# Kernel optimization log

Hardware: AMD Instinct MI355X
Metric: run time of the kernel (lower is better)

## Reference

```python
import jax, jax.numpy as jnp
import numpy as np

B, N, C, H = 4, 2048, 768, 12
D = C // H  # head_dim = 64


def setup_inputs() -> dict:
    key = jax.random.key(0)
    ks = jax.random.split(key, 16)
    s = 1.0 / np.sqrt(C)
    inp = {
        "x1": jax.random.normal(ks[0], (B, N, C), jnp.float32),
        "x2": jax.random.normal(ks[1], (B, N, C), jnp.float32),
        "mask_1": jax.random.uniform(ks[2], (B, N), jnp.float32),
        "mask_2": jax.random.uniform(ks[3], (B, N), jnp.float32),
        "Wq": jax.random.normal(ks[4], (C, C), jnp.float32) * s,
        "bq": jnp.zeros((C,), jnp.float32),
        "Wk": jax.random.normal(ks[5], (C, C), jnp.float32) * s,
        "bk": jnp.zeros((C,), jnp.float32),
        "Wv": jax.random.normal(ks[6], (C, C), jnp.float32) * s,
        "bv": jnp.zeros((C,), jnp.float32),
        "Wo": jax.random.normal(ks[7], (C, C), jnp.float32) * s,
        "bo": jnp.zeros((C,), jnp.float32),
        "temperature": jnp.asarray(1.0, jnp.float32),
        "ln_gamma": jnp.ones((C,), jnp.float32),
        "ln_beta": jnp.zeros((C,), jnp.float32),
    }
    return inp


def _layernorm(x, gamma, beta, eps=1e-5):
    mu = jnp.mean(x, axis=-1, keepdims=True)
    var = jnp.var(x, axis=-1, keepdims=True)
    return (x - mu) * jax.lax.rsqrt(var + eps) * gamma + beta


def reference(x1, x2, mask_1, mask_2, Wq, bq, Wk, bk, Wv, bv, Wo, bo,
              temperature, ln_gamma, ln_beta):
    # projections (nn.Linear: x @ W^T + b)
    q = (x1 @ Wq.T + bq).reshape(B, N, H, D).transpose(0, 2, 1, 3)  # [B,H,N,D]
    k = (x2 @ Wk.T + bk).reshape(B, N, H, D).transpose(0, 2, 1, 3)
    v = (x2 @ Wv.T + bv).reshape(B, N, H, D).transpose(0, 2, 1, 3)

    scores = jnp.einsum("bhnd,bhmd->bhnm", q, k) / jnp.sqrt(jnp.float32(D))
    # relative confidence bias: (mask_1[b,n] - mask_2[b,m]) / temperature
    rel = (mask_1[:, :, None] - mask_2[:, None, :]) / temperature  # [B,N,N]
    scores = scores + rel[:, None, :, :]

    attn = jax.nn.softmax(scores, axis=-1)  # dropout = identity (eval mode)
    out = jnp.einsum("bhnm,bhmd->bhnd", attn, v)
    out = out.transpose(0, 2, 1, 3).reshape(B, N, C)
    out = out @ Wo.T + bo
    return _layernorm(0.5 * x1 + out, ln_gamma, ln_beta)
```

## Files before the change

### kernel.cpp

```cpp
#include <hip/hip_runtime.h>
#include <stdint.h>

#define B_ 4
#define N_ 2048
#define C_ 768
#define H_ 12
#define D_ 64
#define NTOK 8192

typedef short bf16x8 __attribute__((ext_vector_type(8)));
typedef float f32x4 __attribute__((ext_vector_type(4)));
typedef float f32x16 __attribute__((ext_vector_type(16)));
typedef unsigned short ushort8 __attribute__((ext_vector_type(8)));
typedef unsigned short u16x4 __attribute__((ext_vector_type(4)));

__device__ __forceinline__ unsigned short f2bf(float f) {
  union { float f; unsigned u; } v; v.f = f;
  unsigned r = v.u + 0x7FFFu + ((v.u >> 16) & 1u);
  return (unsigned short)(r >> 16);
}

__device__ __forceinline__ void load_lds16(const void* g, void* lds_base) {
  __builtin_amdgcn_global_load_lds(
      (const __attribute__((address_space(1))) unsigned int*)g,
      (__attribute__((address_space(3))) unsigned int*)(uint32_t)(uintptr_t)lds_base,
      16, 0, 0);
}

__device__ __forceinline__ int key2slot(int key) {
  return ((key >> 5) << 5) | (((key >> 4) & 1) << 4) | (((key >> 2) & 1) << 3)
       | (((key >> 3) & 1) << 2) | (key & 3);
}

__device__ __forceinline__ bf16x8 pack8(const float* p) {
  union { unsigned u[4]; bf16x8 v; } r;
#pragma unroll
  for (int j=0;j<4;j++) {
    union { float f; unsigned u; } a, b;
    a.f = p[2*j]; b.f = p[2*j+1];
    r.u[j] = __builtin_amdgcn_perm(b.u + 0x8000u, a.u + 0x8000u, 0x07060302u);
  }
  return r.v;
}

__global__ __launch_bounds__(256) void cvt6(
    const float* s0, const float* s1, const float* s2, const float* s3,
    const float* s4, const float* s5,
    unsigned short* d0, unsigned short* d1, unsigned short* d2,
    unsigned short* d3, unsigned short* d4, unsigned short* d5,
    int n01, int n25)
{
  int y = blockIdx.y;
  const float* s = (y==0)?s0:(y==1)?s1:(y==2)?s2:(y==3)?s3:(y==4)?s4:s5;
  unsigned short* d = (y==0)?d0:(y==1)?d1:(y==2)?d2:(y==3)?d3:(y==4)?d4:d5;
  int n = (y<2) ? n01 : n25;
  int i = (blockIdx.x*256 + threadIdx.x)*8;
  if (i >= n) return;
  float4 f0 = *(const float4*)(s+i);
  float4 f1 = *(const float4*)(s+i+4);
  ushort8 o;
  o[0]=f2bf(f0.x); o[1]=f2bf(f0.y); o[2]=f2bf(f0.z); o[3]=f2bf(f0.w);
  o[4]=f2bf(f1.x); o[5]=f2bf(f1.y); o[6]=f2bf(f1.z); o[7]=f2bf(f1.w);
  *(ushort8*)(d+i) = o;
}

__device__ __forceinline__ void gemm_core(const unsigned short* A, const unsigned short* W,
                                          int rowBase, int colBase, f32x4 (&acc)[4][4],
                                          unsigned short* As, unsigned short* Bs)
{
  int tid = threadIdx.x, wave = tid>>6, lane = tid&63, quad = lane>>4, l16 = lane&15;
  int wm = wave>>1, wn = wave&1;
  for (int k0 = 0; k0 < 768; k0 += 32) {
    __syncthreads();
#pragma unroll
    for (int p = 0; p < 2; ++p) {
      int c = p*256 + wave*64 + lane;
      load_lds16(A + (size_t)(rowBase + (c>>2))*768 + k0 + (c&3)*8,
                 As + (size_t)(p*256 + wave*64)*8);
      load_lds16(W + (size_t)(colBase + (c>>2))*768 + k0 + (c&3)*8,
                 Bs + (size_t)(p*256 + wave*64)*8);
    }
    __syncthreads();
    bf16x8 af[4], bw[4];
#pragma unroll
    for (int i=0;i<4;i++) af[i] = *(const bf16x8*)(As + (wm*64 + i*16 + l16)*32 + quad*8);
#pragma unroll
    for (int j=0;j<4;j++) bw[j] = *(const bf16x8*)(Bs + (wn*64 + j*16 + l16)*32 + quad*8);
#pragma unroll
    for (int i=0;i<4;i++)
#pragma unroll
      for (int j=0;j<4;j++)
        acc[i][j] = __builtin_amdgcn_mfma_f32_16x16x32_bf16(af[i], bw[j], acc[i][j], 0,0,0);
  }
}

__global__ __launch_bounds__(256) void qkv_gemm(
    const unsigned short* xb1, const unsigned short* xb2,
    const unsigned short* Wq, const unsigned short* Wk, const unsigned short* Wv,
    const float* bq, const float* bk, const float* bv,
    unsigned short* Qb, unsigned short* Kb, unsigned short* Vb)
{
  __shared__ unsigned short As[128*32];
  __shared__ unsigned short Bs[128*32];
  int z = blockIdx.z;
  const unsigned short* A = (z==0) ? xb1 : xb2;
  const unsigned short* W = (z==0) ? Wq : (z==1) ? Wk : Wv;
  const float* bias       = (z==0) ? bq : (z==1) ? bk : bv;
  unsigned short* out     = (z==0) ? Qb : (z==1) ? Kb : Vb;
  int rowBase = blockIdx.x*128, colBase = blockIdx.y*128;
  int tid = threadIdx.x, wave = tid>>6, lane = tid&63, quad = lane>>4, l16 = lane&15;
  int wm = wave>>1, wn = wave&1;
  f32x4 acc[4][4] = {};
  gemm_core(A, W, rowBase, colBase, acc, As, Bs);
  if (z == 2) {
#pragma unroll
    for (int i=0;i<4;i++)
#pragma unroll
      for (int j=0;j<4;j++) {
        int col = colBase + wn*64 + j*16 + l16;
        float bv_ = bias[col];
        int h = col >> 6, d = col & 63;
        int m0 = rowBase + wm*64 + i*16 + quad*4;
        int b = m0 >> 11, n0 = m0 & 2047;
        int nslot = (n0 & ~63) | key2slot(n0 & 63);
        u16x4 o;
#pragma unroll
        for (int r=0;r<4;r++) o[r] = f2bf(acc[i][j][r] + bv_);
        *(u16x4*)(out + ((size_t)(b*H_ + h)*D_ + d)*N_ + nslot) = o;
      }
  } else {
#pragma unroll
    for (int i=0;i<4;i++)
#pragma unroll
      for (int j=0;j<4;j++) {
        int col = colBase + wn*64 + j*16 + l16;
        float bv_ = bias[col];
        int h = col >> 6, d = col & 63;
#pragma unroll
        for (int r=0;r<4;r++) {
          int m = rowBase + wm*64 + i*16 + quad*4 + r;
          int b = m >> 11, n = m & 2047;
          out[(((size_t)b*H_ + h)*N_ + n)*D_ + d] = f2bf(acc[i][j][r] + bv_);
        }
      }
  }
}

__device__ __forceinline__ void attn_stage(const unsigned short* Kb, const unsigned short* Vtg,
                                           size_t bh, int kt, int tid, int wave,
                                           unsigned short* KsBuf, unsigned short* VsBuf)
{
#pragma unroll
  for (int p=0;p<2;p++) {
    int idx = p*256 + tid;
    int key = idx >> 3, c = idx & 7;
    load_lds16(Kb + (bh*N_ + (size_t)kt*64 + key)*D_ + (c ^ (key & 7))*8,
               KsBuf + (size_t)(p*256 + wave*64)*8);
  }
#pragma unroll
  for (int p=0;p<2;p++) {
    int idx = p*256 + tid;
    int d = idx >> 3, c = idx & 7;
    load_lds16(Vtg + (bh*D_ + d)*(size_t)N_ + kt*64 + (c ^ (d & 7))*8,
               VsBuf + (size_t)(p*256 + wave*64)*8);
  }
}

__global__ __launch_bounds__(256) void attn_kernel(
    const unsigned short* Qb, const unsigned short* Kb, const unsigned short* Vtg,
    const float* mask2, const float* temp,
    unsigned short* Ob)
{
  __shared__ unsigned short Ks[2][64*64];
  __shared__ unsigned short Vs[2][64*64];
  __shared__ float m2x[N_];
  const float LOG2E = 1.4426950408889634f;
  const float SCL = 0.125f * LOG2E;
  int bx = blockIdx.x;
  int xcd = bx & 7, slot = bx >> 3;
  int bh_i = xcd*6 + (slot >> 4);
  int qt = slot & 15;
  int b = bh_i / H_, h = bh_i - b*H_; (void)h;
  int tid = threadIdx.x, wave = tid>>6, lane = tid&63;
  int l32 = lane & 31, hl = lane >> 5;
  float invT = 1.0f / temp[0];
  size_t bh = (size_t)bh_i;
  int qrow = qt*128 + wave*32 + l32;

#pragma unroll
  for (int r=0;r<8;r++) {
    int i = r*256 + tid;
    m2x[i] = (-mask2[b*N_ + i]*invT - 8.0f) * LOG2E;
  }

  bf16x8 qf[4];
  const unsigned short* Qp = Qb + (bh*N_ + qrow)*D_;
#pragma unroll
  for (int i=0;i<4;i++) qf[i] = *(const bf16x8*)(Qp + i*16 + hl*8);

  float lrun = 0.f;
  f32x16 oacc0 = {}, oacc1 = {};

  attn_stage(Kb, Vtg, bh, 0, tid, wave, Ks[0], Vs[0]);
  __syncthreads();

  for (int kt = 0; kt < N_/64; ++kt) {
    int cur = kt & 1;
    if (kt+1 < N_/64)
      attn_stage(Kb, Vtg, bh, kt+1, tid, wave, Ks[cur^1], Vs[cur^1]);
    const unsigned short* Kc = Ks[cur];
    const unsigned short* Vc = Vs[cur];
#pragma unroll
    for (int sub=0; sub<2; ++sub) {
      f32x16 sa = {};
#pragma unroll
      for (int i=0;i<4;i++) {
        int ch = (2*i + hl) ^ (l32 & 7);
        bf16x8 kf = *(const bf16x8*)(Kc + (sub*32 + l32)*64 + ch*8);
        sa = __builtin_amdgcn_mfma_f32_32x32x16_bf16(kf, qf[i], sa, 0,0,0);
      }
      float pv[16];
#pragma unroll
      for (int g=0; g<4; ++g) {
        float4 mv = *(const float4*)(m2x + kt*64 + sub*32 + g*8 + hl*4);
#pragma unroll
        for (int q=0;q<4;q++)
          pv[g*4+q] = __builtin_amdgcn_exp2f(sa[g*4+q]*SCL + ((const float*)&mv)[q]);
      }
      bf16x8 pf0 = pack8(pv);
      bf16x8 pf1 = pack8(pv+8);
#pragma unroll
      for (int kc=0;kc<2;kc++) {
        bf16x8 pf = kc ? pf1 : pf0;
        int cc = sub*4 + kc*2 + hl;
        {
          int d = l32;
          bf16x8 vf = *(const bf16x8*)(Vc + d*64 + (cc ^ (d&7))*8);
          oacc0 = __builtin_amdgcn_mfma_f32_32x32x16_bf16(vf, pf, oacc0, 0,0,0);
        }
        {
          int d = 32 + l32;
          bf16x8 vf = *(const bf16x8*)(Vc + d*64 + (cc ^ (d&7))*8);
          oacc1 = __builtin_amdgcn_mfma_f32_32x32x16_bf16(vf, pf, oacc1, 0,0,0);
        }
      }
      float rs = 0.f;
#pragma unroll
      for (int r=0;r<16;r++) rs += pv[r];
      lrun += rs;
    }
    __syncthreads();
  }

  lrun += __shfl_xor(lrun, 32);
  float rinv = 1.0f / lrun;
  size_t obase = ((size_t)b*N_ + qrow)*C_ + h*D_;
#pragma unroll
  for (int dh=0; dh<2; ++dh)
#pragma unroll
    for (int g=0; g<4; ++g) {
      int d = dh*32 + g*8 + hl*4;
      u16x4 o;
#pragma unroll
      for (int q=0;q<4;q++) {
        float val = (dh==0 ? oacc0[g*4+q] : oacc1[g*4+q]) * rinv;
        o[q] = f2bf(val);
      }
      *(u16x4*)(Ob + obase + d) = o;
    }
}

__global__ __launch_bounds__(256) void out_gemm(
    const unsigned short* Ob, const unsigned short* Wo, const float* bo,
    const float* x1, float* Z)
{
  __shared__ unsigned short As[128*32];
  __shared__ unsigned short Bs[128*32];
  int rowBase = blockIdx.x*128, colBase = blockIdx.y*128;
  int tid = threadIdx.x, wave = tid>>6, lane = tid&63, quad = lane>>4, l16 = lane&15;
  int wm = wave>>1, wn = wave&1;
  f32x4 acc[4][4] = {};
  gemm_core(Ob, Wo, rowBase, colBase, acc, As, Bs);
#pragma unroll
  for (int i=0;i<4;i++)
#pragma unroll
    for (int j=0;j<4;j++) {
      int col = colBase + wn*64 + j*16 + l16;
      float bv_ = bo[col];
#pragma unroll
      for (int r=0;r<4;r++) {
        size_t m = rowBase + wm*64 + i*16 + quad*4 + r;
        Z[m*768 + col] = acc[i][j][r] + bv_ + 0.5f*x1[m*768 + col];
      }
    }
}

__global__ __launch_bounds__(256) void ln_kernel(const float* Z, const float* gam,
                                                 const float* bet, float* out)
{
  size_t row = blockIdx.x;
  int t = threadIdx.x;
  const float* z = Z + row*768;
  float v0 = z[t], v1 = z[t+256], v2 = z[t+512];
  float s = v0+v1+v2;
  float ss = v0*v0 + v1*v1 + v2*v2;
#pragma unroll
  for (int off=1; off<64; off<<=1) { s += __shfl_xor(s, off); ss += __shfl_xor(ss, off); }
  __shared__ float red[8];
  int wave = t>>6, lane = t&63;
  if (lane==0) { red[wave] = s; red[4+wave] = ss; }
  __syncthreads();
  float S = red[0]+red[1]+red[2]+red[3];
  float SS = red[4]+red[5]+red[6]+red[7];
  float mean = S * (1.0f/768.0f);
  float var = SS * (1.0f/768.0f) - mean*mean;
  float rstd = rsqrtf(var + 1e-5f);
  float* o = out + row*768;
  o[t]     = (v0-mean)*rstd*gam[t]     + bet[t];
  o[t+256] = (v1-mean)*rstd*gam[t+256] + bet[t+256];
  o[t+512] = (v2-mean)*rstd*gam[t+512] + bet[t+512];
}

extern "C" void kernel_launch(void* const* d_in, const int* in_sizes, int n_in,
                              void* d_out, int out_size, void* d_ws, size_t ws_size,
                              hipStream_t stream)
{
  const float* x1    = (const float*)d_in[0];
  const float* x2    = (const float*)d_in[1];
  const float* mask2 = (const float*)d_in[3];
  const float* Wq    = (const float*)d_in[4];
  const float* bq    = (const float*)d_in[5];
  const float* Wk    = (const float*)d_in[6];
  const float* bk    = (const float*)d_in[7];
  const float* Wv    = (const float*)d_in[8];
  const float* bv    = (const float*)d_in[9];
  const float* Wo    = (const float*)d_in[10];
  const float* bo    = (const float*)d_in[11];
  const float* temp  = (const float*)d_in[12];
  const float* gam   = (const float*)d_in[13];
  const float* bet   = (const float*)d_in[14];

  char* ws = (char*)d_ws;
  size_t off = 0;
  auto alloc = [&](size_t bytes) { void* p = ws + off; off += (bytes + 255) & ~255ull; return p; };
  const size_t XB = (size_t)NTOK * C_ * 2;
  const size_t WB = (size_t)C_ * C_ * 2;
  unsigned short* xb1 = (unsigned short*)alloc(XB);
  unsigned short* xb2 = (unsigned short*)alloc(XB);
  unsigned short* Wqb = (unsigned short*)alloc(WB);
  unsigned short* Wkb = (unsigned short*)alloc(WB);
  unsigned short* Wvb = (unsigned short*)alloc(WB);
  unsigned short* Wob = (unsigned short*)alloc(WB);
  unsigned short* Qb  = (unsigned short*)alloc(XB);
  unsigned short* Kb  = (unsigned short*)alloc(XB);
  unsigned short* Vb  = (unsigned short*)alloc(XB);
  unsigned short* Ob  = (unsigned short*)alloc(XB);
  float* Z = (float*)xb1;

  cvt6<<<dim3(3072, 6), 256, 0, stream>>>(x1, x2, Wq, Wk, Wv, Wo,
                                          xb1, xb2, Wqb, Wkb, Wvb, Wob,
                                          NTOK*C_, C_*C_);
  qkv_gemm<<<dim3(64, 6, 3), 256, 0, stream>>>(xb1, xb2, Wqb, Wkb, Wvb,
                                               bq, bk, bv, Qb, Kb, Vb);
  attn_kernel<<<dim3(768), 256, 0, stream>>>(Qb, Kb, Vb, mask2, temp, Ob);
  out_gemm<<<dim3(64, 6), 256, 0, stream>>>(Ob, Wob, bo, x1, Z);
  ln_kernel<<<dim3(8192), 256, 0, stream>>>(Z, gam, bet, (float*)d_out);
}
```

Before: 292.8 us.

## Stage V-projection output through LDS for coalesced stores; precompute attention LDS offsets

The V-projection epilogue now writes the transposed, slot-permuted tile into shared memory and then copies it out as contiguous 16-byte vector stores, replacing the previous scattered 8-byte stores into the D-major layout. In the attention kernel, the swizzled LDS offsets for K and V fragments are computed once into registers and the key loop is unrolled by two, which cuts per-iteration address arithmetic. The epilogue adds two block barriers and reuses the GEMM shared buffer, and the unroll may raise register pressure.

```diff
diff --git a/kernel.cpp b/kernel.cpp
--- a/kernel.cpp
+++ b/kernel.cpp
@@ -100,8 +100,9 @@
     const float* bq, const float* bk, const float* bv,
     unsigned short* Qb, unsigned short* Kb, unsigned short* Vb)
 {
-  __shared__ unsigned short As[128*32];
-  __shared__ unsigned short Bs[128*32];
+  __shared__ unsigned short SU[64*132];
+  unsigned short* As = SU;
+  unsigned short* Bs = SU + 4096;
   int z = blockIdx.z;
   const unsigned short* A = (z==0) ? xb1 : xb2;
   const unsigned short* W = (z==0) ? Wq : (z==1) ? Wk : Wv;
@@ -113,21 +114,35 @@
   f32x4 acc[4][4] = {};
   gemm_core(A, W, rowBase, colBase, acc, As, Bs);
   if (z == 2) {
-#pragma unroll
-    for (int i=0;i<4;i++)
-#pragma unroll
-      for (int j=0;j<4;j++) {
-        int col = colBase + wn*64 + j*16 + l16;
-        float bv_ = bias[col];
-        int h = col >> 6, d = col & 63;
-        int m0 = rowBase + wm*64 + i*16 + quad*4;
-        int b = m0 >> 11, n0 = m0 & 2047;
-        int nslot = (n0 & ~63) | key2slot(n0 & 63);
-        u16x4 o;
-#pragma unroll
-        for (int r=0;r<4;r++) o[r] = f2bf(acc[i][j][r] + bv_);
-        *(u16x4*)(out + ((size_t)(b*H_ + h)*D_ + d)*N_ + nslot) = o;
-      }
+    unsigned short* T = SU;
+    int b = rowBase >> 11, n0 = rowBase & 2047;
+#pragma unroll
+    for (int phase=0; phase<2; ++phase) {
+      __syncthreads();
+      if (wn == phase) {
+#pragma unroll
+        for (int i=0;i<4;i++)
+#pragma unroll
+          for (int j=0;j<4;j++) {
+            int d = j*16 + l16;
+            float bv_ = bias[colBase + phase*64 + d];
+#pragma unroll
+            for (int r=0;r<4;r++) {
+              int t = wm*64 + i*16 + quad*4 + r;
+              int sl = (t & 64) | key2slot(t & 63);
+              T[d*132 + sl] = f2bf(acc[i][j][r] + bv_);
+            }
+          }
+      }
+      __syncthreads();
+      int h = (colBase >> 6) + phase;
+      int row = tid >> 2, seg = tid & 3;
+      unsigned short* dst = out + ((size_t)(b*H_ + h)*D_ + row)*N_ + n0 + seg*32;
+      const unsigned short* src = T + row*132 + seg*32;
+#pragma unroll
+      for (int u=0;u<4;u++)
+        *(ushort8*)(dst + u*8) = *(const ushort8*)(src + u*8);
+    }
   } else {
 #pragma unroll
     for (int i=0;i<4;i++)
@@ -171,8 +186,8 @@
     const float* mask2, const float* temp,
     unsigned short* Ob)
 {
-  __shared__ unsigned short Ks[2][64*64];
-  __shared__ unsigned short Vs[2][64*64];
+  __shared__ unsigned short Ks[2*64*64];
+  __shared__ unsigned short Vs[2*64*64];
   __shared__ float m2x[N_];
   const float LOG2E = 1.4426950408889634f;
   const float SCL = 0.125f * LOG2E;
@@ -180,7 +195,7 @@
   int xcd = bx & 7, slot = bx >> 3;
   int bh_i = xcd*6 + (slot >> 4);
   int qt = slot & 15;
-  int b = bh_i / H_, h = bh_i - b*H_; (void)h;
+  int b = bh_i / H_, h = bh_i - b*H_;
   int tid = threadIdx.x, wave = tid>>6, lane = tid&63;
   int l32 = lane & 31, hl = lane >> 5;
   float invT = 1.0f / temp[0];
@@ -198,25 +213,27 @@
 #pragma unroll
   for (int i=0;i<4;i++) qf[i] = *(const bf16x8*)(Qp + i*16 + hl*8);
 
+  int loff[4];
+#pragma unroll
+  for (int t=0;t<4;t++) loff[t] = l32*64 + (((2*t + hl) ^ (l32 & 7))*8);
+
   float lrun = 0.f;
   f32x16 oacc0 = {}, oacc1 = {};
 
-  attn_stage(Kb, Vtg, bh, 0, tid, wave, Ks[0], Vs[0]);
+  attn_stage(Kb, Vtg, bh, 0, tid, wave, Ks, Vs);
   __syncthreads();
 
+#pragma unroll 2
   for (int kt = 0; kt < N_/64; ++kt) {
     int cur = kt & 1;
     if (kt+1 < N_/64)
-      attn_stage(Kb, Vtg, bh, kt+1, tid, wave, Ks[cur^1], Vs[cur^1]);
-    const unsigned short* Kc = Ks[cur];
-    const unsigned short* Vc = Vs[cur];
+      attn_stage(Kb, Vtg, bh, kt+1, tid, wave, Ks + (cur^1)*4096, Vs + (cur^1)*4096);
 #pragma unroll
     for (int sub=0; sub<2; ++sub) {
       f32x16 sa = {};
 #pragma unroll
       for (int i=0;i<4;i++) {
-        int ch = (2*i + hl) ^ (l32 & 7);
-        bf16x8 kf = *(const bf16x8*)(Kc + (sub*32 + l32)*64 + ch*8);
+        bf16x8 kf = *(const bf16x8*)(Ks + cur*4096 + sub*2048 + loff[i]);
         sa = __builtin_amdgcn_mfma_f32_32x32x16_bf16(kf, qf[i], sa, 0,0,0);
       }
       float pv[16];
@@ -232,17 +249,11 @@
 #pragma unroll
       for (int kc=0;kc<2;kc++) {
         bf16x8 pf = kc ? pf1 : pf0;
-        int cc = sub*4 + kc*2 + hl;
-        {
-          int d = l32;
-          bf16x8 vf = *(const bf16x8*)(Vc + d*64 + (cc ^ (d&7))*8);
-          oacc0 = __builtin_amdgcn_mfma_f32_32x32x16_bf16(vf, pf, oacc0, 0,0,0);
-        }
-        {
-          int d = 32 + l32;
-          bf16x8 vf = *(const bf16x8*)(Vc + d*64 + (cc ^ (d&7))*8);
-          oacc1 = __builtin_amdgcn_mfma_f32_32x32x16_bf16(vf, pf, oacc1, 0,0,0);
-        }
+        int m = sub*2 + kc;
+        oacc0 = __builtin_amdgcn_mfma_f32_32x32x16_bf16(
+                  *(const bf16x8*)(Vs + cur*4096 + loff[m]), pf, oacc0, 0,0,0);
+        oacc1 = __builtin_amdgcn_mfma_f32_32x32x16_bf16(
+                  *(const bf16x8*)(Vs + cur*4096 + 2048 + loff[m]), pf, oacc1, 0,0,0);
       }
       float rs = 0.f;
 #pragma unroll
```

Result: no change. 294.0 us (+0.4%).

## Split V transpose into separate kernel and simplify attention P packing

Applied to the files above, without the earlier changes.

The QKV GEMM now writes V in the same row-major layout as Q and K, and a new vtrans kernel transposes it through LDS into the key-slot-permuted transposed layout that attention expects, reusing the xb2 buffer. This replaces the scattered strided V stores in the GEMM epilogue with coalesced writes. The cost is an extra launch and a full read and write of V. The attention kernel also drops the rounding add in P's bf16 packing, so P is truncated rather than rounded, which slightly changes numerics. It also vectorises the row-sum and rewrites the V fragment index arithmetic.

```diff
diff --git a/kernel.cpp b/kernel.cpp
--- a/kernel.cpp
+++ b/kernel.cpp
@@ -11,6 +11,7 @@
 typedef short bf16x8 __attribute__((ext_vector_type(8)));
 typedef float f32x4 __attribute__((ext_vector_type(4)));
 typedef float f32x16 __attribute__((ext_vector_type(16)));
+typedef float f32x2v __attribute__((ext_vector_type(2)));
 typedef unsigned short ushort8 __attribute__((ext_vector_type(8)));
 typedef unsigned short u16x4 __attribute__((ext_vector_type(4)));
 
@@ -32,13 +33,13 @@
        | (((key >> 3) & 1) << 2) | (key & 3);
 }
 
-__device__ __forceinline__ bf16x8 pack8(const float* p) {
+__device__ __forceinline__ bf16x8 pack8t(const float* p) {
   union { unsigned u[4]; bf16x8 v; } r;
 #pragma unroll
   for (int j=0;j<4;j++) {
     union { float f; unsigned u; } a, b;
     a.f = p[2*j]; b.f = p[2*j+1];
-    r.u[j] = __builtin_amdgcn_perm(b.u + 0x8000u, a.u + 0x8000u, 0x07060302u);
+    r.u[j] = __builtin_amdgcn_perm(b.u, a.u, 0x07060302u);
   }
   return r.v;
 }
@@ -112,38 +113,43 @@
   int wm = wave>>1, wn = wave&1;
   f32x4 acc[4][4] = {};
   gemm_core(A, W, rowBase, colBase, acc, As, Bs);
-  if (z == 2) {
-#pragma unroll
-    for (int i=0;i<4;i++)
-#pragma unroll
-      for (int j=0;j<4;j++) {
-        int col = colBase + wn*64 + j*16 + l16;
-        float bv_ = bias[col];
-        int h = col >> 6, d = col & 63;
-        int m0 = rowBase + wm*64 + i*16 + quad*4;
-        int b = m0 >> 11, n0 = m0 & 2047;
-        int nslot = (n0 & ~63) | key2slot(n0 & 63);
-        u16x4 o;
-#pragma unroll
-        for (int r=0;r<4;r++) o[r] = f2bf(acc[i][j][r] + bv_);
-        *(u16x4*)(out + ((size_t)(b*H_ + h)*D_ + d)*N_ + nslot) = o;
-      }
-  } else {
-#pragma unroll
-    for (int i=0;i<4;i++)
-#pragma unroll
-      for (int j=0;j<4;j++) {
-        int col = colBase + wn*64 + j*16 + l16;
-        float bv_ = bias[col];
-        int h = col >> 6, d = col & 63;
-#pragma unroll
-        for (int r=0;r<4;r++) {
-          int m = rowBase + wm*64 + i*16 + quad*4 + r;
-          int b = m >> 11, n = m & 2047;
-          out[(((size_t)b*H_ + h)*N_ + n)*D_ + d] = f2bf(acc[i][j][r] + bv_);
-        }
-      }
-  }
+#pragma unroll
+  for (int i=0;i<4;i++)
+#pragma unroll
+    for (int j=0;j<4;j++) {
+      int col = colBase + wn*64 + j*16 + l16;
+      float bv_ = bias[col];
+      int h = col >> 6, d = col & 63;
+#pragma unroll
+      for (int r=0;r<4;r++) {
+        int m = rowBase + wm*64 + i*16 + quad*4 + r;
+        int b = m >> 11, n = m & 2047;
+        out[(((size_t)b*H_ + h)*N_ + n)*D_ + d] = f2bf(acc[i][j][r] + bv_);
+      }
+    }
+}
+
+__global__ __launch_bounds__(256) void vtrans(const unsigned short* Vb, unsigned short* Vt)
+{
+  __shared__ unsigned short T[64*72];
+  int nt = blockIdx.x;
+  size_t bh = blockIdx.y;
+  int tid = threadIdx.x;
+#pragma unroll
+  for (int p=0;p<2;p++) {
+    int idx = p*256 + tid;
+    int key = idx >> 3, c = idx & 7;
+    bf16x8 v = *(const bf16x8*)(Vb + (bh*N_ + (size_t)nt*64 + key)*D_ + c*8);
+    int sl = key2slot(key);
+#pragma unroll
+    for (int jj=0;jj<8;jj++) T[(c*8+jj)*72 + sl] = (unsigned short)v[jj];
+  }
+  __syncthreads();
+  int d = tid >> 2, seg = tid & 3;
+  unsigned short* dst = Vt + (bh*D_ + d)*(size_t)N_ + nt*64 + seg*16;
+  const unsigned short* src = T + d*72 + seg*16;
+  *(ushort8*)(dst)     = *(const ushort8*)(src);
+  *(ushort8*)(dst + 8) = *(const ushort8*)(src + 8);
 }
 
 __device__ __forceinline__ void attn_stage(const unsigned short* Kb, const unsigned short* Vtg,
@@ -180,7 +186,7 @@
   int xcd = bx & 7, slot = bx >> 3;
   int bh_i = xcd*6 + (slot >> 4);
   int qt = slot & 15;
-  int b = bh_i / H_, h = bh_i - b*H_; (void)h;
+  int b = bh_i / H_, h = bh_i - b*H_;
   int tid = threadIdx.x, wave = tid>>6, lane = tid&63;
   int l32 = lane & 31, hl = lane >> 5;
   float invT = 1.0f / temp[0];
@@ -227,27 +233,23 @@
         for (int q=0;q<4;q++)
           pv[g*4+q] = __builtin_amdgcn_exp2f(sa[g*4+q]*SCL + ((const float*)&mv)[q]);
       }
-      bf16x8 pf0 = pack8(pv);
-      bf16x8 pf1 = pack8(pv+8);
+      bf16x8 pf0 = pack8t(pv);
+      bf16x8 pf1 = pack8t(pv+8);
 #pragma unroll
       for (int kc=0;kc<2;kc++) {
         bf16x8 pf = kc ? pf1 : pf0;
-        int cc = sub*4 + kc*2 + hl;
-        {
-          int d = l32;
-          bf16x8 vf = *(const bf16x8*)(Vc + d*64 + (cc ^ (d&7))*8);
-          oacc0 = __builtin_amdgcn_mfma_f32_32x32x16_bf16(vf, pf, oacc0, 0,0,0);
-        }
-        {
-          int d = 32 + l32;
-          bf16x8 vf = *(const bf16x8*)(Vc + d*64 + (cc ^ (d&7))*8);
-          oacc1 = __builtin_amdgcn_mfma_f32_32x32x16_bf16(vf, pf, oacc1, 0,0,0);
-        }
-      }
-      float rs = 0.f;
-#pragma unroll
-      for (int r=0;r<16;r++) rs += pv[r];
-      lrun += rs;
+        int m = sub*2 + kc;
+        int chv = (2*m + hl) ^ (l32 & 7);
+        oacc0 = __builtin_amdgcn_mfma_f32_32x32x16_bf16(
+                  *(const bf16x8*)(Vc + l32*64 + chv*8), pf, oacc0, 0,0,0);
+        int chv1 = (2*m + hl) ^ ((32+l32) & 7);
+        oacc1 = __builtin_amdgcn_mfma_f32_32x32x16_bf16(
+                  *(const bf16x8*)(Vc + (32+l32)*64 + chv1*8), pf, oacc1, 0,0,0);
+      }
+      f32x2v rs2 = {0.f, 0.f};
+#pragma unroll
+      for (int r=0;r<8;r++) rs2 += *(const f32x2v*)(pv + 2*r);
+      lrun += rs2[0] + rs2[1];
     }
     __syncthreads();
   }
@@ -355,6 +357,7 @@
   unsigned short* Kb  = (unsigned short*)alloc(XB);
   unsigned short* Vb  = (unsigned short*)alloc(XB);
   unsigned short* Ob  = (unsigned short*)alloc(XB);
+  unsigned short* Vt = xb2;
   float* Z = (float*)xb1;
 
   cvt6<<<dim3(3072, 6), 256, 0, stream>>>(x1, x2, Wq, Wk, Wv, Wo,
@@ -362,7 +365,8 @@
                                           NTOK*C_, C_*C_);
   qkv_gemm<<<dim3(64, 6, 3), 256, 0, stream>>>(xb1, xb2, Wqb, Wkb, Wvb,
                                                bq, bk, bv, Qb, Kb, Vb);
-  attn_kernel<<<dim3(768), 256, 0, stream>>>(Qb, Kb, Vb, mask2, temp, Ob);
+  vtrans<<<dim3(32, 48), 256, 0, stream>>>(Vb, Vt);
+  attn_kernel<<<dim3(768), 256, 0, stream>>>(Qb, Kb, Vt, mask2, temp, Ob);
   out_gemm<<<dim3(64, 6), 256, 0, stream>>>(Ob, Wob, bo, x1, Z);
   ln_kernel<<<dim3(8192), 256, 0, stream>>>(Z, gam, bet, (float*)d_out);
 }
```

Measured after the change: 287.4 us. About the same (-1.8%).
